# Kernel tuning notes

Measured on AMD Instinct MI355X. Metric: run time of the kernel, lower is better.

The kernel has to match this reference:

```python
import jax, jax.numpy as jnp
import numpy as np

WS = 7          # window size
NH = 6          # heads
LN_EPS = 1e-5


def _rel_pos_index(ws):
    coords = np.stack(np.meshgrid(np.arange(ws), np.arange(ws), indexing='ij'))  # (2, ws, ws)
    flat = coords.reshape(2, -1)                       # (2, ws*ws)
    rel = flat[:, :, None] - flat[:, None, :]          # (2, N, N)
    rel = rel.transpose(1, 2, 0).copy()
    rel[:, :, 0] += ws - 1
    rel[:, :, 1] += ws - 1
    rel[:, :, 0] *= 2 * ws - 1
    return jnp.asarray(rel.sum(-1).reshape(-1), dtype=jnp.int32)  # (N*N,)


def _layernorm(x, gamma, beta):
    mu = jnp.mean(x, axis=-1, keepdims=True)
    var = jnp.var(x, axis=-1, keepdims=True)
    return (x - mu) * jax.lax.rsqrt(var + LN_EPS) * gamma + beta


def _window_partition(x, ws):
    B, H, W, C = x.shape
    x = x.reshape(B, H // ws, ws, W // ws, ws, C)
    return x.transpose(0, 1, 3, 2, 4, 5).reshape(-1, ws * ws, C)


def _window_reverse(w, ws, H, W, B):
    C = w.shape[-1]
    x = w.reshape(B, H // ws, W // ws, ws, ws, C)
    return x.transpose(0, 1, 3, 2, 4, 5).reshape(B, H, W, C)


def setup_inputs() -> dict:
    key = jax.random.key(0)
    B, H, W, C = 32, 56, 56, 384
    N, hidden = H * W, 1536
    ks = jax.random.split(key, 9)
    s = 0.02
    return {
        'x':      jax.random.normal(ks[0], (B, N, C), jnp.float32),
        'gamma1': jnp.ones((C,), jnp.float32),
        'beta1':  jnp.zeros((C,), jnp.float32),
        'w_qkv':  jax.random.normal(ks[1], (C, 3 * C), jnp.float32) * s,
        'w_proj': jax.random.normal(ks[2], (C, C), jnp.float32) * s,
        'b_proj': jnp.zeros((C,), jnp.float32),
        'rel_bias': jax.random.normal(ks[3], ((2 * WS - 1) ** 2, NH), jnp.float32) * s,
        'gamma2': jnp.ones((C,), jnp.float32),
        'beta2':  jnp.zeros((C,), jnp.float32),
        'w_fc1':  jax.random.normal(ks[4], (C, hidden), jnp.float32) * s,
        'b_fc1':  jnp.zeros((hidden,), jnp.float32),
        'w_dw':   jax.random.normal(ks[5], (hidden, 1, 3, 3), jnp.float32) * s,
        'b_dw':   jnp.zeros((hidden,), jnp.float32),
        'w_fc2':  jax.random.normal(ks[6], (hidden, C), jnp.float32) * s,
        'b_fc2':  jnp.zeros((C,), jnp.float32),
        'H': H,
        'W': W,
    }


def reference(x, gamma1, beta1, w_qkv, w_proj, b_proj, rel_bias,
              gamma2, beta2, w_fc1, b_fc1, w_dw, b_dw, w_fc2, b_fc2, H, W):
    B, N, C = x.shape
    Nw = WS * WS
    hd = C // NH
    scale = hd ** -0.5

    # ---- window attention branch ----
    shortcut = x
    xn = _layernorm(x, gamma1, beta1)
    xw = _window_partition(xn.reshape(B, H, W, C), WS)      # (Bw, Nw, C)
    Bw = xw.shape[0]
    qkv = (xw @ w_qkv).reshape(Bw, Nw, 3, NH, hd)
    q, k, v = [qkv[:, :, i].transpose(0, 2, 1, 3) for i in range(3)]  # (Bw, NH, Nw, hd)
    attn = jnp.einsum('bhnd,bhmd->bhnm', q, k) * scale
    bias = rel_bias[_rel_pos_index(WS)].reshape(Nw, Nw, NH).transpose(2, 0, 1)
    attn = jax.nn.softmax(attn + bias[None], axis=-1)
    out = jnp.einsum('bhnm,bhmd->bhnd', attn, v).transpose(0, 2, 1, 3).reshape(Bw, Nw, C)
    out = out @ w_proj + b_proj
    x = shortcut + _window_reverse(out, WS, H, W, B).reshape(B, N, C)

    # ---- ConvFFN branch ----
    y = _layernorm(x, gamma2, beta2)
    y = y @ w_fc1 + b_fc1                                    # (B, N, hidden)
    hdim = y.shape[-1]
    y2 = y.transpose(0, 2, 1).reshape(B, hdim, H, W)         # NCHW
    y2 = jax.lax.conv_general_dilated(
        y2, w_dw, window_strides=(1, 1), padding='SAME',
        dimension_numbers=('NCHW', 'OIHW', 'NCHW'),
        feature_group_count=hdim) + b_dw[None, :, None, None]
    y = y2.reshape(B, hdim, N).transpose(0, 2, 1)
    y = jax.nn.gelu(y, approximate=False)
    y = y @ w_fc2 + b_fc2
    return x + y
```

## Files before the change

### kernel.cpp

```cpp
#include <hip/hip_runtime.h>
#include <math.h>


typedef __bf16 bf16x8 __attribute__((ext_vector_type(8)));
typedef float f32x4 __attribute__((ext_vector_type(4)));
typedef unsigned short u16x8 __attribute__((ext_vector_type(8)));

__device__ __forceinline__ float b2f(unsigned short u) {
    union { unsigned int i; float f; } x;
    x.i = ((unsigned int)u) << 16;
    return x.f;
}
__device__ __forceinline__ unsigned short f2b(float f) {
    union { float f; unsigned int i; } x;
    x.f = f;
    unsigned int i = x.i;
    return (unsigned short)((i + 0x7fffu + ((i >> 16) & 1u)) >> 16);
}
__device__ __forceinline__ float rd2(const float* pf, const unsigned short* pb,
                                     long i, int f32) {
    return f32 ? pf[i] : b2f(pb[i]);
}

__global__ void detect_dtype(const unsigned int* __restrict__ gamma1,
                             int* __restrict__ flag)
{
    if (threadIdx.x == 0) flag[0] = (gamma1[0] == 0x3F800000u) ? 1 : 0;
}

__global__ __launch_bounds__(256) void convert_smalls(
    const int* __restrict__ flag,
    const void* g1, const void* b1, const void* bp, const void* g2,
    const void* b2, const void* bf1, const void* wdw, const void* bdw,
    const void* bf2, const void* rb, unsigned short* __restrict__ dst)
{
    int i = blockIdx.x * 256 + threadIdx.x;
    if (i >= 20214) return;
    const int f = flag[0];
    const void* src; long j; int o = i;
    if      (i < 384)   { src = g1;  j = i; }
    else if (i < 768)   { src = b1;  j = i - 384; }
    else if (i < 1152)  { src = bp;  j = i - 768; }
    else if (i < 1536)  { src = g2;  j = i - 1152; }
    else if (i < 1920)  { src = b2;  j = i - 1536; }
    else if (i < 3456)  { src = bf1; j = i - 1920; }
    else if (i < 17280) {
        int d = i - 3456, k = d / 1536, ch = d % 1536;
        src = wdw; j = (long)ch * 9 + k;
    }
    else if (i < 18816) { src = bdw; j = i - 17280; }
    else if (i < 19200) { src = bf2; j = i - 18816; }
    else                { src = rb;  j = i - 19200; }
    float v = f ? ((const float*)src)[j] : b2f(((const unsigned short*)src)[j]);
    dst[o] = f2b(v);
}

__global__ __launch_bounds__(256) void transpose_any(
    const void* __restrict__ in, unsigned short* __restrict__ out,
    int R, int C, const int* __restrict__ flag)
{
    __shared__ unsigned short tile[32][33];
    const int f = flag[0];
    int tx = threadIdx.x & 31, ty = threadIdx.x >> 5;
    int rb = blockIdx.y * 32, cb = blockIdx.x * 32;
#pragma unroll
    for (int i = 0; i < 32; i += 8) {
        int r = rb + ty + i, c = cb + tx;
        if (r < R && c < C)
            tile[ty + i][tx] = f2b(rd2((const float*)in,
                                       (const unsigned short*)in,
                                       (long)r * C + c, f));
    }
    __syncthreads();
#pragma unroll
    for (int i = 0; i < 32; i += 8) {
        int c = cb + ty + i, r = rb + tx;
        if (c < C && r < R) out[(long)c * R + r] = tile[tx][ty + i];
    }
}

__global__ __launch_bounds__(256) void ln_kernel(
    const float* __restrict__ xf, const unsigned short* __restrict__ xb,
    const unsigned short* __restrict__ gamma,
    const unsigned short* __restrict__ beta,
    unsigned short* __restrict__ yout, int T,
    const int* __restrict__ flagp, int force_f32)
{
    int w = blockIdx.x * 4 + (threadIdx.x >> 6);
    int lane = threadIdx.x & 63;
    if (w >= T) return;
    const int f32 = force_f32 ? 1 : flagp[0];
    long base = (long)w * 384;
    float v[6];
    float s = 0.f;
#pragma unroll
    for (int i = 0; i < 6; ++i) {
        v[i] = rd2(xf, xb, base + lane + i * 64, f32);
        s += v[i];
    }
#pragma unroll
    for (int o = 32; o > 0; o >>= 1) s += __shfl_xor(s, o);
    float mu = s * (1.f / 384.f);
    float q = 0.f;
#pragma unroll
    for (int i = 0; i < 6; ++i) { float d = v[i] - mu; q += d * d; }
#pragma unroll
    for (int o = 32; o > 0; o >>= 1) q += __shfl_xor(q, o);
    float rs = rsqrtf(q * (1.f / 384.f) + 1e-5f);
#pragma unroll
    for (int i = 0; i < 6; ++i) {
        int cc = lane + i * 64;
        yout[base + cc] = f2b((v[i] - mu) * rs * b2f(gamma[cc]) + b2f(beta[cc]));
    }
}

template<int EPI, bool OUT_F32_S, bool RES_F32_S>
__global__ __launch_bounds__(256) void gemm_nt(
    const unsigned short* __restrict__ A,
    const unsigned short* __restrict__ BT,
    float* __restrict__ Cf, unsigned short* __restrict__ Cb,
    const unsigned short* __restrict__ bias,
    const float* __restrict__ Rf, const unsigned short* __restrict__ Rb,
    int M, int N, int K,
    const int* __restrict__ rflagp, const int* __restrict__ oflagp)
{
    __shared__ __align__(16) unsigned short ldsA[128 * 32];
    __shared__ __align__(16) unsigned short ldsB[128 * 32];
    const int tid = threadIdx.x;
    const int lane = tid & 63;
    const int wv = tid >> 6;
    const int waveM = wv >> 1, waveN = wv & 1;
    const long m0 = (long)blockIdx.x * 128;
    const long n0 = (long)blockIdx.y * 128;

    f32x4 acc[4][4] = {};

    const int c0 = tid, c1 = 256 + tid;
    const int r0 = c0 >> 2, q0 = (c0 & 3) ^ (r0 & 3);
    const int r1 = c1 >> 2, q1 = (c1 & 3) ^ (r1 & 3);
    long am0 = m0 + r0; if (am0 >= M) am0 = M - 1;
    long am1 = m0 + r1; if (am1 >= M) am1 = M - 1;
    const unsigned short* a0p = A + am0 * (long)K + q0 * 8;
    const unsigned short* a1p = A + am1 * (long)K + q1 * 8;
    const unsigned short* b0p = BT + (n0 + r0) * (long)K + q0 * 8;
    const unsigned short* b1p = BT + (n0 + r1) * (long)K + q1 * 8;

    const int rq = lane & 15, quad = lane >> 4;

    for (int kt = 0; kt < K; kt += 32) {
        __builtin_amdgcn_global_load_lds(
            (const __attribute__((address_space(1))) void*)(a0p + kt),
            (__attribute__((address_space(3))) void*)(ldsA + c0 * 8), 16, 0, 0);
        __builtin_amdgcn_global_load_lds(
            (const __attribute__((address_space(1))) void*)(a1p + kt),
            (__attribute__((address_space(3))) void*)(ldsA + c1 * 8), 16, 0, 0);
        __builtin_amdgcn_global_load_lds(
            (const __attribute__((address_space(1))) void*)(b0p + kt),
            (__attribute__((address_space(3))) void*)(ldsB + c0 * 8), 16, 0, 0);
        __builtin_amdgcn_global_load_lds(
            (const __attribute__((address_space(1))) void*)(b1p + kt),
            (__attribute__((address_space(3))) void*)(ldsB + c1 * 8), 16, 0, 0);
        __syncthreads();

        bf16x8 af[4], bfv[4];
#pragma unroll
        for (int mi = 0; mi < 4; ++mi) {
            int R = waveM * 64 + mi * 16 + rq;
            int ch = R * 4 + (quad ^ (R & 3));
            af[mi] = *(const bf16x8*)(ldsA + ch * 8);
        }
#pragma unroll
        for (int ni = 0; ni < 4; ++ni) {
            int R = waveN * 64 + ni * 16 + rq;
            int ch = R * 4 + (quad ^ (R & 3));
            bfv[ni] = *(const bf16x8*)(ldsB + ch * 8);
        }
#pragma unroll
        for (int mi = 0; mi < 4; ++mi)
#pragma unroll
            for (int ni = 0; ni < 4; ++ni)
                acc[mi][ni] = __builtin_amdgcn_mfma_f32_16x16x32_bf16(
                    af[mi], bfv[ni], acc[mi][ni], 0, 0, 0);
        __syncthreads();
    }

    const int res_f32 = rflagp ? rflagp[0] : (RES_F32_S ? 1 : 0);
    const int out_f32 = oflagp ? oflagp[0] : (OUT_F32_S ? 1 : 0);

    const int rq4 = (lane >> 4) * 4;
    const int coln = lane & 15;
#pragma unroll
    for (int mi = 0; mi < 4; ++mi) {
#pragma unroll
        for (int ni = 0; ni < 4; ++ni) {
            long col = n0 + waveN * 64 + ni * 16 + coln;
            float bv = (EPI >= 1) ? b2f(bias[col]) : 0.f;
#pragma unroll
            for (int r = 0; r < 4; ++r) {
                long row = m0 + waveM * 64 + mi * 16 + rq4 + r;
                if (row >= M) continue;
                long off = row * (long)N + col;
                float v = acc[mi][ni][r] + bv;
                if (EPI == 2) v += rd2(Rf, Rb, off, res_f32);
                if (out_f32) Cf[off] = v;
                else Cb[off] = f2b(v);
            }
        }
    }
}

__global__ __launch_bounds__(64) void attn_kernel(
    const unsigned short* __restrict__ qkv,
    const unsigned short* __restrict__ rel_bias,
    unsigned short* __restrict__ out)
{
    __shared__ __align__(16) unsigned short k_lds[64 * 72];
    __shared__ __align__(16) unsigned short v_lds[64 * 72];
    __shared__ __align__(16) unsigned short q_lds[64 * 72];

    const int w = blockIdx.x, hh = blockIdx.y;
    const int lane = threadIdx.x;
    const int b = w >> 6, wh = (w >> 3) & 7, ww = w & 7;
    const long base = (long)b * 3136;
    const unsigned short* src = qkv + hh * 64;

#pragma unroll
    for (int it = 0; it < 13; ++it) {
        int idx = it * 64 + lane;
        if (idx < 784) {
            int t = idx >> 4, d4 = (idx & 15) << 2;
            int pi = t / 7, pj = t % 7;
            const unsigned short* gp =
                src + (base + (wh * 7 + pi) * 56 + (ww * 7 + pj)) * 1152 + d4;
            *(ushort4*)(q_lds + t * 72 + d4) = *(const ushort4*)(gp);
            *(ushort4*)(k_lds + t * 72 + d4) = *(const ushort4*)(gp + 384);
        }
    }
    for (int p = 0; p < 49; ++p) {
        int pi = p / 7, pj = p % 7;
        v_lds[lane * 72 + p] =
            src[(base + (wh * 7 + pi) * 56 + (ww * 7 + pj)) * 1152 + 768 + lane];
    }
#pragma unroll
    for (int p = 49; p < 64; ++p) v_lds[lane * 72 + p] = 0;
    __syncthreads();

    const int rq = lane & 15, quad = lane >> 4;

    bf16x8 kf[4][2], qf[4][2];
#pragma unroll
    for (int t4 = 0; t4 < 4; ++t4)
#pragma unroll
        for (int ks = 0; ks < 2; ++ks) {
            kf[t4][ks] = *(const bf16x8*)(k_lds + (t4 * 16 + rq) * 72 + ks * 32 + quad * 8);
            qf[t4][ks] = *(const bf16x8*)(q_lds + (t4 * 16 + rq) * 72 + ks * 32 + quad * 8);
        }
    f32x4 sa[4][4] = {};
#pragma unroll
    for (int ks = 0; ks < 2; ++ks)
#pragma unroll
        for (int mi = 0; mi < 4; ++mi)
#pragma unroll
            for (int ni = 0; ni < 4; ++ni)
                sa[mi][ni] = __builtin_amdgcn_mfma_f32_16x16x32_bf16(
                    kf[mi][ks], qf[ni][ks], sa[mi][ni], 0, 0, 0);

    const int kq = quad * 4;
#pragma unroll
    for (int ni = 0; ni < 4; ++ni) {
        int q = ni * 16 + rq;
        int qc = (q < 49) ? q : 48;
        int yi = qc / 7, xi = qc % 7;
        float mx = -1e30f;
#pragma unroll
        for (int mi = 0; mi < 4; ++mi)
#pragma unroll
            for (int r = 0; r < 4; ++r) {
                int key = mi * 16 + kq + r;
                float s;
                if (key < 49) {
                    int yj = key / 7, xj = key % 7;
                    int idx = (yi - yj + 6) * 13 + (xi - xj + 6);
                    s = 0.125f * sa[mi][ni][r] + b2f(rel_bias[idx * 6 + hh]);
                } else s = -1e30f;
                sa[mi][ni][r] = s;
                mx = fmaxf(mx, s);
            }
        mx = fmaxf(mx, __shfl_xor(mx, 16));
        mx = fmaxf(mx, __shfl_xor(mx, 32));
        float sum = 0.f;
#pragma unroll
        for (int mi = 0; mi < 4; ++mi)
#pragma unroll
            for (int r = 0; r < 4; ++r) {
                float e = __expf(sa[mi][ni][r] - mx);
                sa[mi][ni][r] = e;
                sum += e;
            }
        sum += __shfl_xor(sum, 16);
        sum += __shfl_xor(sum, 32);
        float rinv = 1.f / sum;
#pragma unroll
        for (int mi = 0; mi < 4; ++mi) {
            unsigned int w0 = (unsigned int)f2b(sa[mi][ni][0] * rinv) |
                              ((unsigned int)f2b(sa[mi][ni][1] * rinv) << 16);
            unsigned int w1 = (unsigned int)f2b(sa[mi][ni][2] * rinv) |
                              ((unsigned int)f2b(sa[mi][ni][3] * rinv) << 16);
            *(unsigned int*)(q_lds + q * 72 + mi * 16 + kq)     = w0;
            *(unsigned int*)(q_lds + q * 72 + mi * 16 + kq + 2) = w1;
        }
    }
    __syncthreads();

    f32x4 oa[4][4] = {};
#pragma unroll
    for (int ks = 0; ks < 2; ++ks) {
        bf16x8 pf[4], vf[4];
#pragma unroll
        for (int qt = 0; qt < 4; ++qt)
            pf[qt] = *(const bf16x8*)(q_lds + (qt * 16 + rq) * 72 + ks * 32 + quad * 8);
#pragma unroll
        for (int dt = 0; dt < 4; ++dt)
            vf[dt] = *(const bf16x8*)(v_lds + (dt * 16 + rq) * 72 + ks * 32 + quad * 8);
#pragma unroll
        for (int qt = 0; qt < 4; ++qt)
#pragma unroll
            for (int dt = 0; dt < 4; ++dt)
                oa[qt][dt] = __builtin_amdgcn_mfma_f32_16x16x32_bf16(
                    pf[qt], vf[dt], oa[qt][dt], 0, 0, 0);
    }

#pragma unroll
    for (int qt = 0; qt < 4; ++qt)
#pragma unroll
        for (int r = 0; r < 4; ++r) {
            int q = qt * 16 + quad * 4 + r;
            if (q >= 49) continue;
            int yi = q / 7, xi = q % 7;
            long t = base + (long)(wh * 7 + yi) * 56 + (ww * 7 + xi);
            unsigned short* op = out + t * 384 + hh * 64;
#pragma unroll
            for (int dt = 0; dt < 4; ++dt)
                op[dt * 16 + rq] = f2b(oa[qt][dt][r]);
        }
}

__global__ __launch_bounds__(192) void dwconv_gelu(
    const unsigned short* __restrict__ h,
    const unsigned short* __restrict__ w_dwT,
    const unsigned short* __restrict__ b_dw,
    unsigned short* __restrict__ g)
{
    const long t = blockIdx.x;
    const int bb = (int)(t / 3136), n = (int)(t % 3136);
    const int r = n / 56, c = n % 56;
    const int ch = threadIdx.x * 8;

    float a[8];
    u16x8 bv = *(const u16x8*)(b_dw + ch);
#pragma unroll
    for (int i = 0; i < 8; ++i) a[i] = b2f(bv[i]);

#pragma unroll
    for (int dr = -1; dr <= 1; ++dr) {
        int rr = r + dr;
        if (rr < 0 || rr >= 56) continue;
#pragma unroll
        for (int dc = -1; dc <= 1; ++dc) {
            int cc = c + dc;
            if (cc < 0 || cc >= 56) continue;
            int k = (dr + 1) * 3 + (dc + 1);
            long off = ((long)bb * 3136 + rr * 56 + cc) * 1536 + ch;
            u16x8 hv = *(const u16x8*)(h + off);
            u16x8 wv = *(const u16x8*)(w_dwT + k * 1536 + ch);
#pragma unroll
            for (int i = 0; i < 8; ++i) a[i] += b2f(hv[i]) * b2f(wv[i]);
        }
    }
    u16x8 ov;
#pragma unroll
    for (int i = 0; i < 8; ++i) {
        float v = 0.5f * a[i] * (1.f + erff(a[i] * 0.70710678118654752f));
        ov[i] = f2b(v);
    }
    *(u16x8*)(g + t * 1536 + ch) = ov;
}

extern "C" void kernel_launch(void* const* d_in, const int* in_sizes, int n_in,
                              void* d_out, int out_size, void* d_ws, size_t ws_size,
                              hipStream_t stream)
{
    const void* x      = d_in[0];
    const void* gamma1 = d_in[1];
    const void* beta1  = d_in[2];
    const void* w_qkv  = d_in[3];
    const void* w_proj = d_in[4];
    const void* b_proj = d_in[5];
    const void* relb   = d_in[6];
    const void* gamma2 = d_in[7];
    const void* beta2  = d_in[8];
    const void* w_fc1  = d_in[9];
    const void* b_fc1  = d_in[10];
    const void* w_dw   = d_in[11];
    const void* b_dw   = d_in[12];
    const void* w_fc2  = d_in[13];
    const void* b_fc2  = d_in[14];

    const int NIMG = 32, NPI = 3136;

    int* flag = (int*)d_ws;
    unsigned short* smalls = (unsigned short*)((char*)d_ws + 16);
    unsigned short* wqkvT  = (unsigned short*)((char*)d_ws + 16 + 20224 * 2);
    unsigned short* wprojT = wqkvT + 1152 * 384;
    unsigned short* wfc1T  = wprojT + 384 * 384;
    unsigned short* wfc2T  = wfc1T + 1536 * 384;
    const size_t WB = 16 + 20224 * 2 +
        ((size_t)1152 * 384 + 384 * 384 + 1536 * 384 + 384 * 1536) * 2;
    char* chunk_base = (char*)d_ws + WB;

    const unsigned short* c_g1   = smalls;
    const unsigned short* c_b1   = smalls + 384;
    const unsigned short* c_bp   = smalls + 768;
    const unsigned short* c_g2   = smalls + 1152;
    const unsigned short* c_b2   = smalls + 1536;
    const unsigned short* c_bf1  = smalls + 1920;
    const unsigned short* c_wdwT = smalls + 3456;
    const unsigned short* c_bdw  = smalls + 17280;
    const unsigned short* c_bf2  = smalls + 18816;
    const unsigned short* c_rb   = smalls + 19200;

    const size_t PER_IMG = (size_t)NPI * 384 * 4 + 2 * (size_t)NPI * 1536 * 2;
    int ipc = NIMG;
    while (ipc > 1 && WB + PER_IMG * (size_t)ipc > ws_size) ipc >>= 1;

    detect_dtype<<<1, 64, 0, stream>>>((const unsigned int*)gamma1, flag);
    convert_smalls<<<80, 256, 0, stream>>>(flag, gamma1, beta1, b_proj, gamma2,
        beta2, b_fc1, w_dw, b_dw, b_fc2, relb, smalls);
    transpose_any<<<dim3(36, 12), 256, 0, stream>>>(w_qkv, wqkvT, 384, 1152, flag);
    transpose_any<<<dim3(12, 12), 256, 0, stream>>>(w_proj, wprojT, 384, 384, flag);
    transpose_any<<<dim3(48, 12), 256, 0, stream>>>(w_fc1, wfc1T, 384, 1536, flag);
    transpose_any<<<dim3(12, 48), 256, 0, stream>>>(w_fc2, wfc2T, 1536, 384, flag);

    for (int i0 = 0; i0 < NIMG; i0 += ipc) {
        const int Tc = ipc * NPI;
        const long tb = (long)i0 * NPI;
        const int GM = (Tc + 127) / 128;

        float* x1 = (float*)chunk_base;
        unsigned short* r1 = (unsigned short*)(chunk_base + (size_t)Tc * 384 * 4);
        unsigned short* r2 = r1 + (size_t)Tc * 1536;

        unsigned short* xn      = r1;
        unsigned short* hbuf    = r1;
        unsigned short* qkv     = r2;
        unsigned short* attnout = r2 + (size_t)Tc * 1152;
        unsigned short* ybuf    = r2;
        unsigned short* gbuf    = r2;

        const float* xf = (const float*)x + tb * 384;
        const unsigned short* xb = (const unsigned short*)x + tb * 384;
        float* of = (float*)d_out + tb * 384;
        unsigned short* ob = (unsigned short*)d_out + tb * 384;

        ln_kernel<<<Tc / 4, 256, 0, stream>>>(xf, xb, c_g1, c_b1, xn, Tc, flag, 0);
        gemm_nt<0, false, false><<<dim3(GM, 9), 256, 0, stream>>>(
            xn, wqkvT, nullptr, qkv, nullptr, nullptr, nullptr,
            Tc, 1152, 384, nullptr, nullptr);
        attn_kernel<<<dim3(ipc * 64, 6), 64, 0, stream>>>(qkv, c_rb, attnout);
        gemm_nt<2, true, false><<<dim3(GM, 3), 256, 0, stream>>>(
            attnout, wprojT, x1, nullptr, c_bp, xf, xb,
            Tc, 384, 384, flag, nullptr);

        ln_kernel<<<Tc / 4, 256, 0, stream>>>(x1, nullptr, c_g2, c_b2, ybuf, Tc,
                                              flag, 1);
        gemm_nt<1, false, false><<<dim3(GM, 12), 256, 0, stream>>>(
            ybuf, wfc1T, nullptr, hbuf, c_bf1, nullptr, nullptr,
            Tc, 1536, 384, nullptr, nullptr);
        dwconv_gelu<<<Tc, 192, 0, stream>>>(hbuf, c_wdwT, c_bdw, gbuf);
        gemm_nt<2, false, true><<<dim3(GM, 3), 256, 0, stream>>>(
            gbuf, wfc2T, of, ob, c_bf2, x1, nullptr,
            Tc, 384, 1536, nullptr, flag);
    }
}
```

Measured before the change: 2.109 ms.

## Double-buffer GEMM K-tiles via register prefetch and remap blocks across XCDs

Rewrites the GEMM main loop to use a K-tile of 64 with two LDS buffers. The next tile is loaded from global into registers while MFMAs run on the current one, replacing the synchronous global_load_lds path. The launch grid is flattened to 1D and block IDs are remapped so consecutive tiles land on the same XCD for L2 reuse. This doubles LDS use to 64KB per block and adds register pressure, which may reduce occupancy.

```diff
diff --git a/kernel.cpp b/kernel.cpp
--- a/kernel.cpp
+++ b/kernel.cpp
@@ -124,64 +124,94 @@
     int M, int N, int K,
     const int* __restrict__ rflagp, const int* __restrict__ oflagp)
 {
-    __shared__ __align__(16) unsigned short ldsA[128 * 32];
-    __shared__ __align__(16) unsigned short ldsB[128 * 32];
+    __shared__ __align__(16) unsigned short ldsA[2][128 * 64];
+    __shared__ __align__(16) unsigned short ldsB[2][128 * 64];
     const int tid = threadIdx.x;
     const int lane = tid & 63;
     const int wv = tid >> 6;
     const int waveM = wv >> 1, waveN = wv & 1;
-    const long m0 = (long)blockIdx.x * 128;
-    const long n0 = (long)blockIdx.y * 128;
+
+    const int nwg = (int)gridDim.x;
+    const int orig = (int)blockIdx.x;
+    const int qq = nwg >> 3, rr = nwg & 7, xcd = orig & 7;
+    const int wgid = (xcd < rr ? xcd * (qq + 1)
+                               : rr * (qq + 1) + (xcd - rr) * qq) + (orig >> 3);
+    const int NB = N >> 7;
+    const long m0 = (long)(wgid / NB) * 128;
+    const long n0 = (long)(wgid % NB) * 128;
 
     f32x4 acc[4][4] = {};
 
-    const int c0 = tid, c1 = 256 + tid;
-    const int r0 = c0 >> 2, q0 = (c0 & 3) ^ (r0 & 3);
-    const int r1 = c1 >> 2, q1 = (c1 & 3) ^ (r1 & 3);
-    long am0 = m0 + r0; if (am0 >= M) am0 = M - 1;
-    long am1 = m0 + r1; if (am1 >= M) am1 = M - 1;
-    const unsigned short* a0p = A + am0 * (long)K + q0 * 8;
-    const unsigned short* a1p = A + am1 * (long)K + q1 * 8;
-    const unsigned short* b0p = BT + (n0 + r0) * (long)K + q0 * 8;
-    const unsigned short* b1p = BT + (n0 + r1) * (long)K + q1 * 8;
-
+    const unsigned short* aptr[4];
+    const unsigned short* bptr[4];
+#pragma unroll
+    for (int i = 0; i < 4; ++i) {
+        int c = tid + i * 256, r = c >> 3, q = (c & 7) ^ (r & 7);
+        long row = m0 + r; if (row >= M) row = M - 1;
+        aptr[i] = A + row * (long)K + q * 8;
+        bptr[i] = BT + (n0 + r) * (long)K + q * 8;
+    }
+
+    u16x8 sa0, sa1, sa2, sa3, sb0, sb1, sb2, sb3;
+
+    auto LOADG = [&](int kt) {
+        sa0 = *(const u16x8*)(aptr[0] + kt);
+        sa1 = *(const u16x8*)(aptr[1] + kt);
+        sa2 = *(const u16x8*)(aptr[2] + kt);
+        sa3 = *(const u16x8*)(aptr[3] + kt);
+        sb0 = *(const u16x8*)(bptr[0] + kt);
+        sb1 = *(const u16x8*)(bptr[1] + kt);
+        sb2 = *(const u16x8*)(bptr[2] + kt);
+        sb3 = *(const u16x8*)(bptr[3] + kt);
+    };
+    auto WRITE = [&](int buf) {
+        *(u16x8*)(&ldsA[buf][(tid          ) * 8]) = sa0;
+        *(u16x8*)(&ldsA[buf][(tid + 1 * 256) * 8]) = sa1;
+        *(u16x8*)(&ldsA[buf][(tid + 2 * 256) * 8]) = sa2;
+        *(u16x8*)(&ldsA[buf][(tid + 3 * 256) * 8]) = sa3;
+        *(u16x8*)(&ldsB[buf][(tid          ) * 8]) = sb0;
+        *(u16x8*)(&ldsB[buf][(tid + 1 * 256) * 8]) = sb1;
+        *(u16x8*)(&ldsB[buf][(tid + 2 * 256) * 8]) = sb2;
+        *(u16x8*)(&ldsB[buf][(tid + 3 * 256) * 8]) = sb3;
+    };
+
+    const int nt = K >> 6;
     const int rq = lane & 15, quad = lane >> 4;
 
-    for (int kt = 0; kt < K; kt += 32) {
-        __builtin_amdgcn_global_load_lds(
-            (const __attribute__((address_space(1))) void*)(a0p + kt),
-            (__attribute__((address_space(3))) void*)(ldsA + c0 * 8), 16, 0, 0);
-        __builtin_amdgcn_global_load_lds(
-            (const __attribute__((address_space(1))) void*)(a1p + kt),
-            (__attribute__((address_space(3))) void*)(ldsA + c1 * 8), 16, 0, 0);
-        __builtin_amdgcn_global_load_lds(
-            (const __attribute__((address_space(1))) void*)(b0p + kt),
-            (__attribute__((address_space(3))) void*)(ldsB + c0 * 8), 16, 0, 0);
-        __builtin_amdgcn_global_load_lds(
-            (const __attribute__((address_space(1))) void*)(b1p + kt),
-            (__attribute__((address_space(3))) void*)(ldsB + c1 * 8), 16, 0, 0);
+    LOADG(0);
+    WRITE(0);
+
+    int cur = 0;
+    for (int t = 0; t < nt; ++t) {
         __syncthreads();
-
-        bf16x8 af[4], bfv[4];
-#pragma unroll
-        for (int mi = 0; mi < 4; ++mi) {
-            int R = waveM * 64 + mi * 16 + rq;
-            int ch = R * 4 + (quad ^ (R & 3));
-            af[mi] = *(const bf16x8*)(ldsA + ch * 8);
-        }
-#pragma unroll
-        for (int ni = 0; ni < 4; ++ni) {
-            int R = waveN * 64 + ni * 16 + rq;
-            int ch = R * 4 + (quad ^ (R & 3));
-            bfv[ni] = *(const bf16x8*)(ldsB + ch * 8);
-        }
-#pragma unroll
-        for (int mi = 0; mi < 4; ++mi)
-#pragma unroll
-            for (int ni = 0; ni < 4; ++ni)
-                acc[mi][ni] = __builtin_amdgcn_mfma_f32_16x16x32_bf16(
-                    af[mi], bfv[ni], acc[mi][ni], 0, 0, 0);
+        if (t + 1 < nt) LOADG((t + 1) * 64);
+
+        const unsigned short* As = ldsA[cur];
+        const unsigned short* Bs = ldsB[cur];
+#pragma unroll
+        for (int h = 0; h < 2; ++h) {
+            bf16x8 av[4], bv[4];
+#pragma unroll
+            for (int mi = 0; mi < 4; ++mi) {
+                int R = waveM * 64 + mi * 16 + rq;
+                av[mi] = *(const bf16x8*)(As + (R * 8 + ((h * 4 + quad) ^ (R & 7))) * 8);
+            }
+#pragma unroll
+            for (int ni = 0; ni < 4; ++ni) {
+                int R = waveN * 64 + ni * 16 + rq;
+                bv[ni] = *(const bf16x8*)(Bs + (R * 8 + ((h * 4 + quad) ^ (R & 7))) * 8);
+            }
+#pragma unroll
+            for (int mi = 0; mi < 4; ++mi)
+#pragma unroll
+                for (int ni = 0; ni < 4; ++ni)
+                    acc[mi][ni] = __builtin_amdgcn_mfma_f32_16x16x32_bf16(
+                        av[mi], bv[ni], acc[mi][ni], 0, 0, 0);
+        }
+
         __syncthreads();
+        if (t + 1 < nt) WRITE(cur ^ 1);
+        cur ^= 1;
     }
 
     const int res_f32 = rflagp ? rflagp[0] : (RES_F32_S ? 1 : 0);
@@ -463,21 +493,21 @@
         unsigned short* ob = (unsigned short*)d_out + tb * 384;
 
         ln_kernel<<<Tc / 4, 256, 0, stream>>>(xf, xb, c_g1, c_b1, xn, Tc, flag, 0);
-        gemm_nt<0, false, false><<<dim3(GM, 9), 256, 0, stream>>>(
+        gemm_nt<0, false, false><<<GM * 9, 256, 0, stream>>>(
             xn, wqkvT, nullptr, qkv, nullptr, nullptr, nullptr,
             Tc, 1152, 384, nullptr, nullptr);
         attn_kernel<<<dim3(ipc * 64, 6), 64, 0, stream>>>(qkv, c_rb, attnout);
-        gemm_nt<2, true, false><<<dim3(GM, 3), 256, 0, stream>>>(
+        gemm_nt<2, true, false><<<GM * 3, 256, 0, stream>>>(
             attnout, wprojT, x1, nullptr, c_bp, xf, xb,
             Tc, 384, 384, flag, nullptr);
 
         ln_kernel<<<Tc / 4, 256, 0, stream>>>(x1, nullptr, c_g2, c_b2, ybuf, Tc,
                                               flag, 1);
-        gemm_nt<1, false, false><<<dim3(GM, 12), 256, 0, stream>>>(
+        gemm_nt<1, false, false><<<GM * 12, 256, 0, stream>>>(
             ybuf, wfc1T, nullptr, hbuf, c_bf1, nullptr, nullptr,
             Tc, 1536, 384, nullptr, nullptr);
         dwconv_gelu<<<Tc, 192, 0, stream>>>(hbuf, c_wdwT, c_bdw, gbuf);
-        gemm_nt<2, false, true><<<dim3(GM, 3), 256, 0, stream>>>(
+        gemm_nt<2, false, true><<<GM * 3, 256, 0, stream>>>(
             gbuf, wfc2T, of, ob, c_bf2, x1, nullptr,
             Tc, 384, 1536, nullptr, flag);
     }
```

Measured after the change: 1.917 ms. 1.1x faster.
